# Optimization experiments

Hardware: AMD Instinct MI355X
Metric: run time of the kernel (lower is better)

Reference implementation:

```python
import jax, jax.numpy as jnp
import numpy as np

NEG = -1.0e9  # masked_fill value from the original module

def setup_inputs() -> dict:
    key = jax.random.key(0)
    kq, kk, kv, km = jax.random.split(key, 4)
    B, H, S, D = 4, 16, 2048, 64
    Q = jax.random.normal(kq, (B, H, S, D), dtype=jnp.float32)
    K = jax.random.normal(kk, (B, H, S, D), dtype=jnp.float32)
    V = jax.random.normal(kv, (B, H, S, D), dtype=jnp.float32)
    # boolean mask, True = masked out (broadcast over batch and heads)
    mask = jax.random.randint(km, (1, 1, S, S), 0, 2).astype(jnp.bool_)
    return {"Q": Q, "K": K, "V": V, "mask": mask}

def reference(Q, K, V, mask):
    d_k = K.shape[-1]
    scale = 1.0 / jnp.sqrt(jnp.asarray(d_k, dtype=Q.dtype))
    # [B,H,S,S] attention scores
    scores = jnp.einsum("bhqd,bhkd->bhqk", Q, K) * scale
    scores = jnp.where(mask, jnp.asarray(NEG, dtype=scores.dtype), scores)
    weights = jax.nn.softmax(scores, axis=-1)
    # dropout is identity in eval mode (self.training == False)
    return jnp.einsum("bhqk,bhkd->bhqd", weights, V)
```

## Files before the change

kernel.cpp:

```cpp
#include <hip/hip_runtime.h>
#include <stdint.h>

#define SQ 2048
#define DH 64

typedef __attribute__((ext_vector_type(8))) short bf16x8;
typedef __attribute__((ext_vector_type(4))) short bf16x4;
typedef __attribute__((ext_vector_type(4))) float f32x4;

static __device__ __forceinline__ unsigned short f2bf_rne(float x) {
  union { float f; uint32_t u; } v; v.f = x;
  uint32_t u = v.u;
  return (unsigned short)((u + 0x7FFFu + ((u >> 16) & 1u)) >> 16);
}

static __device__ __forceinline__ uint32_t pack_hi(float a, float b) {
  uint32_t au = __float_as_uint(a), bu = __float_as_uint(b);
#if __has_builtin(__builtin_amdgcn_perm)
  return __builtin_amdgcn_perm(bu, au, 0x07060302u);
#else
  return (bu & 0xFFFF0000u) | (au >> 16);
#endif
}

static __device__ __forceinline__ float fast_exp2(float x) {
#if __has_builtin(__builtin_amdgcn_exp2f)
  return __builtin_amdgcn_exp2f(x);
#else
  return exp2f(x);
#endif
}

#if __has_builtin(__builtin_amdgcn_mfma_f32_16x16x16_bf16)
#define MFMA_PV(a, b, c) __builtin_amdgcn_mfma_f32_16x16x16_bf16((a), (b), (c), 0, 0, 0)
#else
#define MFMA_PV(a, b, c) __builtin_amdgcn_mfma_f32_16x16x16bf16_1k((a), (b), (c), 0, 0, 0)
#endif


__global__ __launch_bounds__(256) void pack_KV(const float* __restrict__ K,
                                               const float* __restrict__ V,
                                               uint4* __restrict__ pk,
                                               uint2* __restrict__ pv) {
  __shared__ uint32_t Vw[64][33];
  const int bt = blockIdx.x;
  const int t = threadIdx.x;
  {
    const float* src = K + (size_t)bt * 64 * DH;
    uint4* dst = pk + (size_t)bt * 512;
#pragma unroll
    for (int j = 0; j < 2; ++j) {
      int i = t + j * 256;
      int kk = i >> 3, cp = i & 7;
      int c = cp ^ (kk & 7);
      const float4* s4 = (const float4*)(src + (size_t)kk * DH + c * 8);
      float4 a = s4[0], b = s4[1];
      uint4 w;
      w.x = pack_hi(a.x, a.y); w.y = pack_hi(a.z, a.w);
      w.z = pack_hi(b.x, b.y); w.w = pack_hi(b.z, b.w);
      dst[i] = w;
    }
  }
  {
    const float* src = V + (size_t)bt * 64 * DH;
#pragma unroll
    for (int half = 0; half < 2; ++half) {
      int kp = (t >> 4) + half * 16;
      int d4 = (t & 15) * 4;
      float4 a = *(const float4*)(src + (size_t)(2 * kp) * DH + d4);
      float4 b = *(const float4*)(src + (size_t)(2 * kp + 1) * DH + d4);
      Vw[d4 + 0][kp] = pack_hi(a.x, b.x);
      Vw[d4 + 1][kp] = pack_hi(a.y, b.y);
      Vw[d4 + 2][kp] = pack_hi(a.z, b.z);
      Vw[d4 + 3][kp] = pack_hi(a.w, b.w);
    }
    __syncthreads();
    uint2* dst = pv + (size_t)bt * 1024;
#pragma unroll
    for (int j = 0; j < 4; ++j) {
      int o = t + j * 256;
      int d = o >> 4, up = o & 15;
      int u = up ^ (d & 15);
      uint2 w;
      w.x = Vw[d][2 * u]; w.y = Vw[d][2 * u + 1];
      dst[o] = w;
    }
  }
}

__global__ __launch_bounds__(256) void pack_M(const int* __restrict__ mask,
                                              uint2* __restrict__ pm) {
  __shared__ uint2 Lm[16][17];
  const int qb = blockIdx.x >> 5, gb = blockIdx.x & 31;
  const int t = threadIdx.x;
  {
    int qq = t >> 4, gg = t & 15;
    int4 m = *(const int4*)(mask + (size_t)(qb * 16 + qq) * SQ + (gb * 16 + gg) * 4);
    uint2 w;
    w.x = (m.x ? 0u : 0xFFFFu) | (m.y ? 0u : 0xFFFF0000u);
    w.y = (m.z ? 0u : 0xFFFFu) | (m.w ? 0u : 0xFFFF0000u);
    Lm[gg][qq] = w;
  }
  __syncthreads();
  {
    int gg = t >> 4, qq = t & 15;
    pm[(size_t)(gb * 16 + gg) * 2048 + qb * 16 + qq] = Lm[gg][qq];
  }
}

__global__ void pack_mask_kernel(const int* __restrict__ mask,
                                 unsigned long long* __restrict__ bits) {
  const int lane = threadIdx.x & 63;
  const int gw = (blockIdx.x * blockDim.x + threadIdx.x) >> 6;
  const int nw = (gridDim.x * blockDim.x) >> 6;
  for (int w = gw; w < SQ * SQ / 64; w += nw) {
    int v = mask[(size_t)w * 64 + lane];
    unsigned long long b = __ballot(v != 0);
    if (lane == 0) bits[(size_t)(w & 31) * SQ + (w >> 5)] = b;
  }
}

__global__ __launch_bounds__(256, 4) void attn2(
    const uint4* __restrict__ pk, const uint4* __restrict__ pv,
    const uint2* __restrict__ pm, const float* __restrict__ Qg,
    float* __restrict__ Og) {
  __shared__ __align__(16) uint8_t smem[32768];

  const int id = blockIdx.x;
  const int bh = id & 63;
  const int qblk = id >> 6;
  const int t = threadIdx.x;
  const int wave = t >> 6, lane = t & 63, col = lane & 15, quad = lane >> 4;

  const float* Qb = Qg + (size_t)bh * SQ * DH;
  float* Ob = Og + (size_t)bh * SQ * DH;
  const uint4* pkb = pk + (size_t)bh * 32 * 512;
  const uint4* pvb = pv + (size_t)bh * 32 * 512;
  const int q0 = qblk * 128 + wave * 32;

  const float QSCALE = 0.18033688011112042f;
  bf16x8 qf[2][2];
#pragma unroll
  for (int s = 0; s < 2; ++s) {
    int q = q0 + s * 16 + col;
#pragma unroll
    for (int j = 0; j < 2; ++j) {
      const float4* p = (const float4*)(Qb + (size_t)q * DH + j * 32 + quad * 8);
      float4 a = p[0], b = p[1];
      bf16x8 f;
      f[0] = (short)f2bf_rne(a.x * QSCALE); f[1] = (short)f2bf_rne(a.y * QSCALE);
      f[2] = (short)f2bf_rne(a.z * QSCALE); f[3] = (short)f2bf_rne(a.w * QSCALE);
      f[4] = (short)f2bf_rne(b.x * QSCALE); f[5] = (short)f2bf_rne(b.y * QSCALE);
      f[6] = (short)f2bf_rne(b.z * QSCALE); f[7] = (short)f2bf_rne(b.w * QSCALE);
      qf[s][j] = f;
    }
  }

  const unsigned ka0 = col * 128 + ((quad ^ (col & 7)) * 16);
  const unsigned ka1 = col * 128 + (((4 + quad) ^ (col & 7)) * 16);
  unsigned va[4];
#pragma unroll
  for (int kt = 0; kt < 4; ++kt)
    va[kt] = 16384u + col * 128 + (((kt * 4 + quad) ^ col) * 8);
  const unsigned stK = t * 16;
  const unsigned stV = 16384u + t * 16;
  const size_t mqB = (size_t)(quad * 2048 + q0 + col) * 8;

  f32x4 acc[2][4];
  f32x4 accl[2];
#pragma unroll
  for (int s = 0; s < 2; ++s) {
#pragma unroll
    for (int dt = 0; dt < 4; ++dt)
#pragma unroll
      for (int r = 0; r < 4; ++r) acc[s][dt][r] = 0.0f;
#pragma unroll
    for (int r = 0; r < 4; ++r) accl[s][r] = 0.0f;
  }
  bf16x4 vones;
  vones[0] = (short)0x3F80; vones[1] = (short)0x3F80;
  vones[2] = (short)0x3F80; vones[3] = (short)0x3F80;
  const f32x4 fz = {0.0f, 0.0f, 0.0f, 0.0f};

  {
    uint4 k0 = pkb[t], k1 = pkb[t + 256];
    uint4 v0 = pvb[t], v1 = pvb[t + 256];
    *(uint4*)(smem + stK) = k0; *(uint4*)(smem + stK + 4096) = k1;
    *(uint4*)(smem + stV) = v0; *(uint4*)(smem + stV + 4096) = v1;
  }
  unsigned buf = 0;

  for (int tile = 0; tile < 32; ++tile) {
    __syncthreads();
    const int tn = (tile < 31) ? tile + 1 : 31;

    const uint4* pkt = pkb + (size_t)tn * 512;
    const uint4* pvt = pvb + (size_t)tn * 512;
    uint4 k0 = pkt[t], k1 = pkt[t + 256];
    uint4 v0 = pvt[t], v1 = pvt[t + 256];

    const char* pmt = (const char*)pm + (size_t)tile * 262144 + mqB;
    uint2 mw[2][4];
#pragma unroll
    for (int s = 0; s < 2; ++s)
#pragma unroll
      for (int kt = 0; kt < 4; ++kt)
        mw[s][kt] = *(const uint2*)(pmt + (size_t)kt * 65536 + s * 128);

    uint32_t pfw[2][4][2];
#pragma unroll
    for (int kt = 0; kt < 4; ++kt) {
      const bf16x8 kf0 = *(const bf16x8*)(smem + buf + ka0 + kt * 2048);
      const bf16x8 kf1 = *(const bf16x8*)(smem + buf + ka1 + kt * 2048);
#pragma unroll
      for (int s = 0; s < 2; ++s) {
        f32x4 st = __builtin_amdgcn_mfma_f32_16x16x32_bf16(kf0, qf[s][0], fz, 0, 0, 0);
        st = __builtin_amdgcn_mfma_f32_16x16x32_bf16(kf1, qf[s][1], st, 0, 0, 0);
        float p0 = fast_exp2(st[0]), p1 = fast_exp2(st[1]);
        float p2 = fast_exp2(st[2]), p3 = fast_exp2(st[3]);
        pfw[s][kt][0] = pack_hi(p0, p1) & mw[s][kt].x;
        pfw[s][kt][1] = pack_hi(p2, p3) & mw[s][kt].y;
      }
    }

#pragma unroll
    for (int kt = 0; kt < 4; ++kt) {
      union { uint32_t u[2]; bf16x4 v; } p0, p1;
      p0.u[0] = pfw[0][kt][0]; p0.u[1] = pfw[0][kt][1];
      p1.u[0] = pfw[1][kt][0]; p1.u[1] = pfw[1][kt][1];
      accl[0] = MFMA_PV(vones, p0.v, accl[0]);
      accl[1] = MFMA_PV(vones, p1.v, accl[1]);
#pragma unroll
      for (int dt = 0; dt < 4; ++dt) {
        union { uint2 u2; bf16x4 v; } cv;
        cv.u2 = *(const uint2*)(smem + buf + va[kt] + dt * 2048);
        acc[0][dt] = MFMA_PV(cv.v, p0.v, acc[0][dt]);
        acc[1][dt] = MFMA_PV(cv.v, p1.v, acc[1][dt]);
      }
    }

    const unsigned ob = buf ^ 8192u;
    *(uint4*)(smem + ob + stK) = k0; *(uint4*)(smem + ob + stK + 4096) = k1;
    *(uint4*)(smem + ob + stV) = v0; *(uint4*)(smem + ob + stV + 4096) = v1;
    buf = ob;
  }

#pragma unroll
  for (int s = 0; s < 2; ++s) {
    float inv = 1.0f / accl[s][0];
    int q = q0 + s * 16 + col;
    float* orow = Ob + (size_t)q * DH;
#pragma unroll
    for (int dt = 0; dt < 4; ++dt) {
      float4 o;
      o.x = acc[s][dt][0] * inv;
      o.y = acc[s][dt][1] * inv;
      o.z = acc[s][dt][2] * inv;
      o.w = acc[s][dt][3] * inv;
      *(float4*)(orow + dt * 16 + quad * 4) = o;
    }
  }
}

__global__ __launch_bounds__(512, 4) void attn_fb(
    const float* __restrict__ Qg, const float* __restrict__ Kg,
    const float* __restrict__ Vg, const unsigned long long* __restrict__ mbits,
    const int* __restrict__ mraw, float* __restrict__ Og) {
  __shared__ __align__(16) unsigned short Klds[2][64][72];
  __shared__ __align__(16) uint32_t Vtlds[2][64][36];
  const int id = blockIdx.x;
  const int bh = id & 63;
  const int qblk = id >> 6;
  const int t = threadIdx.x;
  const int wave = t >> 6, lane = t & 63, col = lane & 15, quad = lane >> 4;
  const float* Qb = Qg + (size_t)bh * SQ * DH;
  const float* Kb = Kg + (size_t)bh * SQ * DH;
  const float* Vb = Vg + (size_t)bh * SQ * DH;
  float* Ob = Og + (size_t)bh * SQ * DH;
  const int q0 = qblk * 256 + wave * 32;
  const int skk = t >> 3, sd8 = (t & 7) * 8, skp = t >> 4, sd4 = (t & 15) * 4;
  const float QSCALE = 0.18033688011112042f;
  bf16x8 qf[2][2];
#pragma unroll
  for (int s = 0; s < 2; ++s) {
    int q = q0 + s * 16 + col;
#pragma unroll
    for (int j = 0; j < 2; ++j) {
      const float4* p = (const float4*)(Qb + (size_t)q * DH + j * 32 + quad * 8);
      float4 a = p[0], b = p[1];
      bf16x8 f;
      f[0] = (short)f2bf_rne(a.x * QSCALE); f[1] = (short)f2bf_rne(a.y * QSCALE);
      f[2] = (short)f2bf_rne(a.z * QSCALE); f[3] = (short)f2bf_rne(a.w * QSCALE);
      f[4] = (short)f2bf_rne(b.x * QSCALE); f[5] = (short)f2bf_rne(b.y * QSCALE);
      f[6] = (short)f2bf_rne(b.z * QSCALE); f[7] = (short)f2bf_rne(b.w * QSCALE);
      qf[s][j] = f;
    }
  }
  f32x4 acc[2][4]; f32x4 accl[2];
#pragma unroll
  for (int s = 0; s < 2; ++s) {
#pragma unroll
    for (int dt = 0; dt < 4; ++dt)
#pragma unroll
      for (int r = 0; r < 4; ++r) acc[s][dt][r] = 0.0f;
#pragma unroll
    for (int r = 0; r < 4; ++r) accl[s][r] = 0.0f;
  }
  bf16x4 vones;
  vones[0] = (short)0x3F80; vones[1] = (short)0x3F80;
  vones[2] = (short)0x3F80; vones[3] = (short)0x3F80;
  const f32x4 fz = {0.0f, 0.0f, 0.0f, 0.0f};
  auto load_mask = [&](int ti, unsigned long long m[2]) {
    if (mbits) {
#pragma unroll
      for (int s = 0; s < 2; ++s)
        m[s] = mbits[(size_t)ti * SQ + (q0 + s * 16 + col)];
    } else {
#pragma unroll
      for (int s = 0; s < 2; ++s) {
        int q = q0 + s * 16 + col;
        unsigned long long mm = 0;
#pragma unroll
        for (int j = 0; j < 4; ++j) {
          int4 mi = *(const int4*)(mraw + (size_t)q * SQ + ti * 64 + j * 16 + quad * 4);
          unsigned long long nib = (unsigned long long)((mi.x != 0) | ((mi.y != 0) << 1) |
                                                        ((mi.z != 0) << 2) | ((mi.w != 0) << 3));
          mm |= nib << (j * 16 + quad * 4);
        }
        m[s] = mm;
      }
    }
  };
  {
    const float4* kp = (const float4*)(Kb + (size_t)skk * DH + sd8);
    float4 k0 = kp[0], k1 = kp[1];
    const float* va = Vb + (size_t)(skp * 2) * DH + sd4;
    float4 v0 = *(const float4*)va, v1 = *(const float4*)(va + DH);
    uint4 kw;
    kw.x = pack_hi(k0.x, k0.y); kw.y = pack_hi(k0.z, k0.w);
    kw.z = pack_hi(k1.x, k1.y); kw.w = pack_hi(k1.z, k1.w);
    *(uint4*)&Klds[0][skk][sd8] = kw;
    Vtlds[0][sd4 + 0][skp] = pack_hi(v0.x, v1.x);
    Vtlds[0][sd4 + 1][skp] = pack_hi(v0.y, v1.y);
    Vtlds[0][sd4 + 2][skp] = pack_hi(v0.z, v1.z);
    Vtlds[0][sd4 + 3][skp] = pack_hi(v0.w, v1.w);
  }
  unsigned long long mcur[2];
  load_mask(0, mcur);
  for (int tile = 0; tile < 32; ++tile) {
    __syncthreads();
    const int cb = tile & 1, nb = cb ^ 1;
    const int tn = (tile + 1 < 32) ? tile + 1 : tile;
    const int kkn = tn * 64;
    const float4* kp = (const float4*)(Kb + (size_t)(kkn + skk) * DH + sd8);
    float4 k0 = kp[0], k1 = kp[1];
    const float* va = Vb + (size_t)(kkn + skp * 2) * DH + sd4;
    float4 v0 = *(const float4*)va;
    float4 v1 = *(const float4*)(va + DH);
    unsigned long long mnxt[2];
    load_mask(tn, mnxt);
    uint32_t pfw[2][4][2];
#pragma unroll
    for (int kt = 0; kt < 4; ++kt) {
      const bf16x8 kf0 = *(const bf16x8*)&Klds[cb][kt * 16 + col][quad * 8];
      const bf16x8 kf1 = *(const bf16x8*)&Klds[cb][kt * 16 + col][32 + quad * 8];
#pragma unroll
      for (int s = 0; s < 2; ++s) {
        f32x4 st = __builtin_amdgcn_mfma_f32_16x16x32_bf16(kf0, qf[s][0], fz, 0, 0, 0);
        st = __builtin_amdgcn_mfma_f32_16x16x32_bf16(kf1, qf[s][1], st, 0, 0, 0);
        uint32_t nib = (uint32_t)(mcur[s] >> (kt * 16 + quad * 4)) & 0xFu;
        float p[4];
#pragma unroll
        for (int r = 0; r < 4; ++r)
          p[r] = fast_exp2(((nib >> r) & 1u) ? -1.0e9f : st[r]);
        pfw[s][kt][0] = pack_hi(p[0], p[1]);
        pfw[s][kt][1] = pack_hi(p[2], p[3]);
      }
    }
    {
      uint4 kw;
      kw.x = pack_hi(k0.x, k0.y); kw.y = pack_hi(k0.z, k0.w);
      kw.z = pack_hi(k1.x, k1.y); kw.w = pack_hi(k1.z, k1.w);
      *(uint4*)&Klds[nb][skk][sd8] = kw;
      Vtlds[nb][sd4 + 0][skp] = pack_hi(v0.x, v1.x);
      Vtlds[nb][sd4 + 1][skp] = pack_hi(v0.y, v1.y);
      Vtlds[nb][sd4 + 2][skp] = pack_hi(v0.z, v1.z);
      Vtlds[nb][sd4 + 3][skp] = pack_hi(v0.w, v1.w);
    }
    mcur[0] = mnxt[0]; mcur[1] = mnxt[1];
#pragma unroll
    for (int kt = 0; kt < 4; ++kt) {
      union { uint32_t u[2]; bf16x4 v; } p0, p1;
      p0.u[0] = pfw[0][kt][0]; p0.u[1] = pfw[0][kt][1];
      p1.u[0] = pfw[1][kt][0]; p1.u[1] = pfw[1][kt][1];
      accl[0] = MFMA_PV(vones, p0.v, accl[0]);
      accl[1] = MFMA_PV(vones, p1.v, accl[1]);
#pragma unroll
      for (int dt = 0; dt < 4; ++dt) {
        union { uint2 u2; bf16x4 v; } cv;
        cv.u2 = *(const uint2*)&Vtlds[cb][dt * 16 + col][kt * 8 + quad * 2];
        acc[0][dt] = MFMA_PV(cv.v, p0.v, acc[0][dt]);
        acc[1][dt] = MFMA_PV(cv.v, p1.v, acc[1][dt]);
      }
    }
  }
#pragma unroll
  for (int s = 0; s < 2; ++s) {
    float inv = 1.0f / accl[s][0];
    int q = q0 + s * 16 + col;
    float* orow = Ob + (size_t)q * DH;
#pragma unroll
    for (int dt = 0; dt < 4; ++dt) {
      float4 o;
      o.x = acc[s][dt][0] * inv;
      o.y = acc[s][dt][1] * inv;
      o.z = acc[s][dt][2] * inv;
      o.w = acc[s][dt][3] * inv;
      *(float4*)(orow + dt * 16 + quad * 4) = o;
    }
  }
}

extern "C" void kernel_launch(void* const* d_in, const int* in_sizes, int n_in,
                              void* d_out, int out_size, void* d_ws, size_t ws_size,
                              hipStream_t stream) {
  const float* Q = (const float*)d_in[0];
  const float* K = (const float*)d_in[1];
  const float* V = (const float*)d_in[2];
  const int* mask = (const int*)d_in[3];
  float* out = (float*)d_out;

  const size_t PK_BYTES = (size_t)64 * 32 * 8192;
  const size_t PV_BYTES = (size_t)64 * 32 * 8192;
  const size_t PM_BYTES = (size_t)512 * 2048 * 8;
  const size_t NEED = PK_BYTES + PV_BYTES + PM_BYTES;

  if (ws_size >= NEED) {
    uint4* pk = (uint4*)d_ws;
    uint2* pv = (uint2*)((char*)d_ws + PK_BYTES);
    uint2* pm = (uint2*)((char*)d_ws + PK_BYTES + PV_BYTES);
    pack_KV<<<2048, 256, 0, stream>>>(K, V, pk, (uint2*)pv);
    pack_M<<<4096, 256, 0, stream>>>(mask, pm);
    attn2<<<1024, 256, 0, stream>>>(pk, (uint4*)pv, pm, Q, out);
  } else if (ws_size >= (size_t)SQ * SQ / 8) {
    unsigned long long* bits = (unsigned long long*)d_ws;
    pack_mask_kernel<<<1024, 256, 0, stream>>>(mask, bits);
    attn_fb<<<512, 512, 0, stream>>>(Q, K, V, bits, mask, out);
  } else {
    attn_fb<<<512, 512, 0, stream>>>(Q, K, V, nullptr, mask, out);
  }
}
```

Measured before the change: 242.8 us.

## Double query rows per wave, fuse pack kernels, encode mask as perm selectors

Each wave now handles 64 query rows instead of 32, so every K/V tile loaded into shared memory is reused across twice as many rows. The grid drops to 512 blocks and launch bounds go to 2 blocks per CU to make room for the larger accumulator set. The K/V packing and mask packing kernels are merged into one launch, which removes a launch and its gap. The mask is now stored as byte-permute selectors, so a single perm instruction both packs the probabilities to bf16 and zeroes masked entries, replacing a pack followed by an AND. The risks are higher register pressure and lower occupancy, and a 512-block grid may not fill every CU evenly.

```diff
diff --git a/kernel.cpp b/kernel.cpp
--- a/kernel.cpp
+++ b/kernel.cpp
@@ -23,6 +23,21 @@
 #endif
 }
 
+static __device__ __forceinline__ uint32_t pack_sel(float a, float b, uint32_t sel) {
+#if __has_builtin(__builtin_amdgcn_perm)
+  return __builtin_amdgcn_perm(__float_as_uint(b), __float_as_uint(a), sel);
+#else
+  uint32_t r = 0;
+  uint64_t src = ((uint64_t)__float_as_uint(b) << 32) | __float_as_uint(a);
+  for (int i = 0; i < 4; ++i) {
+    uint32_t sb = (sel >> (8 * i)) & 0xFF;
+    uint32_t byte = (sb < 8) ? (uint32_t)((src >> (8 * sb)) & 0xFF) : 0u;
+    r |= byte << (8 * i);
+  }
+  return r;
+#endif
+}
+
 static __device__ __forceinline__ float fast_exp2(float x) {
 #if __has_builtin(__builtin_amdgcn_exp2f)
   return __builtin_amdgcn_exp2f(x);
@@ -37,74 +52,74 @@
 #define MFMA_PV(a, b, c) __builtin_amdgcn_mfma_f32_16x16x16bf16_1k((a), (b), (c), 0, 0, 0)
 #endif
 
-
-__global__ __launch_bounds__(256) void pack_KV(const float* __restrict__ K,
-                                               const float* __restrict__ V,
-                                               uint4* __restrict__ pk,
-                                               uint2* __restrict__ pv) {
-  __shared__ uint32_t Vw[64][33];
-  const int bt = blockIdx.x;
+__global__ __launch_bounds__(256) void pack_all(const float* __restrict__ K,
+                                                const float* __restrict__ V,
+                                                const int* __restrict__ mask,
+                                                uint4* __restrict__ pk,
+                                                uint2* __restrict__ pv,
+                                                uint2* __restrict__ pm) {
   const int t = threadIdx.x;
-  {
-    const float* src = K + (size_t)bt * 64 * DH;
-    uint4* dst = pk + (size_t)bt * 512;
-#pragma unroll
-    for (int j = 0; j < 2; ++j) {
-      int i = t + j * 256;
-      int kk = i >> 3, cp = i & 7;
-      int c = cp ^ (kk & 7);
-      const float4* s4 = (const float4*)(src + (size_t)kk * DH + c * 8);
-      float4 a = s4[0], b = s4[1];
-      uint4 w;
-      w.x = pack_hi(a.x, a.y); w.y = pack_hi(a.z, a.w);
-      w.z = pack_hi(b.x, b.y); w.w = pack_hi(b.z, b.w);
-      dst[i] = w;
-    }
-  }
-  {
-    const float* src = V + (size_t)bt * 64 * DH;
-#pragma unroll
-    for (int half = 0; half < 2; ++half) {
-      int kp = (t >> 4) + half * 16;
-      int d4 = (t & 15) * 4;
-      float4 a = *(const float4*)(src + (size_t)(2 * kp) * DH + d4);
-      float4 b = *(const float4*)(src + (size_t)(2 * kp + 1) * DH + d4);
-      Vw[d4 + 0][kp] = pack_hi(a.x, b.x);
-      Vw[d4 + 1][kp] = pack_hi(a.y, b.y);
-      Vw[d4 + 2][kp] = pack_hi(a.z, b.z);
-      Vw[d4 + 3][kp] = pack_hi(a.w, b.w);
+  if (blockIdx.x < 2048) {
+    __shared__ uint32_t Vw[64][33];
+    const int bt = blockIdx.x;
+    {
+      const float* src = K + (size_t)bt * 64 * DH;
+      uint4* dst = pk + (size_t)bt * 512;
+#pragma unroll
+      for (int j = 0; j < 2; ++j) {
+        int i = t + j * 256;
+        int kk = i >> 3, cp = i & 7;
+        int c = cp ^ (kk & 7);
+        const float4* s4 = (const float4*)(src + (size_t)kk * DH + c * 8);
+        float4 a = s4[0], b = s4[1];
+        uint4 w;
+        w.x = pack_hi(a.x, a.y); w.y = pack_hi(a.z, a.w);
+        w.z = pack_hi(b.x, b.y); w.w = pack_hi(b.z, b.w);
+        dst[i] = w;
+      }
+    }
+    {
+      const float* src = V + (size_t)bt * 64 * DH;
+#pragma unroll
+      for (int half = 0; half < 2; ++half) {
+        int kp = (t >> 4) + half * 16;
+        int d4 = (t & 15) * 4;
+        float4 a = *(const float4*)(src + (size_t)(2 * kp) * DH + d4);
+        float4 b = *(const float4*)(src + (size_t)(2 * kp + 1) * DH + d4);
+        Vw[d4 + 0][kp] = pack_hi(a.x, b.x);
+        Vw[d4 + 1][kp] = pack_hi(a.y, b.y);
+        Vw[d4 + 2][kp] = pack_hi(a.z, b.z);
+        Vw[d4 + 3][kp] = pack_hi(a.w, b.w);
+      }
+      __syncthreads();
+      uint2* dst = pv + (size_t)bt * 1024;
+#pragma unroll
+      for (int j = 0; j < 4; ++j) {
+        int o = t + j * 256;
+        int d = o >> 4, up = o & 15;
+        int u = up ^ (d & 15);
+        uint2 w;
+        w.x = Vw[d][2 * u]; w.y = Vw[d][2 * u + 1];
+        dst[o] = w;
+      }
+    }
+  } else {
+    __shared__ uint2 Lm[16][17];
+    const int bid = blockIdx.x - 2048;
+    const int qb = bid >> 5, gb = bid & 31;
+    {
+      int qq = t >> 4, gg = t & 15;
+      int4 m = *(const int4*)(mask + (size_t)(qb * 16 + qq) * SQ + (gb * 64 + gg * 4));
+      uint2 w;
+      w.x = (m.x ? 0x00000C0Cu : 0x00000302u) | (m.y ? 0x0C0C0000u : 0x07060000u);
+      w.y = (m.z ? 0x00000C0Cu : 0x00000302u) | (m.w ? 0x0C0C0000u : 0x07060000u);
+      Lm[gg][qq] = w;
     }
     __syncthreads();
-    uint2* dst = pv + (size_t)bt * 1024;
-#pragma unroll
-    for (int j = 0; j < 4; ++j) {
-      int o = t + j * 256;
-      int d = o >> 4, up = o & 15;
-      int u = up ^ (d & 15);
-      uint2 w;
-      w.x = Vw[d][2 * u]; w.y = Vw[d][2 * u + 1];
-      dst[o] = w;
-    }
-  }
-}
-
-__global__ __launch_bounds__(256) void pack_M(const int* __restrict__ mask,
-                                              uint2* __restrict__ pm) {
-  __shared__ uint2 Lm[16][17];
-  const int qb = blockIdx.x >> 5, gb = blockIdx.x & 31;
-  const int t = threadIdx.x;
-  {
-    int qq = t >> 4, gg = t & 15;
-    int4 m = *(const int4*)(mask + (size_t)(qb * 16 + qq) * SQ + (gb * 16 + gg) * 4);
-    uint2 w;
-    w.x = (m.x ? 0u : 0xFFFFu) | (m.y ? 0u : 0xFFFF0000u);
-    w.y = (m.z ? 0u : 0xFFFFu) | (m.w ? 0u : 0xFFFF0000u);
-    Lm[gg][qq] = w;
-  }
-  __syncthreads();
-  {
-    int gg = t >> 4, qq = t & 15;
-    pm[(size_t)(gb * 16 + gg) * 2048 + qb * 16 + qq] = Lm[gg][qq];
+    {
+      int gg = t >> 4, qq = t & 15;
+      pm[(size_t)(gb * 16 + gg) * 2048 + qb * 16 + qq] = Lm[gg][qq];
+    }
   }
 }
 
@@ -120,7 +135,7 @@
   }
 }
 
-__global__ __launch_bounds__(256, 4) void attn2(
+__global__ __launch_bounds__(256, 2) void attn3(
     const uint4* __restrict__ pk, const uint4* __restrict__ pv,
     const uint2* __restrict__ pm, const float* __restrict__ Qg,
     float* __restrict__ Og) {
@@ -136,12 +151,12 @@
   float* Ob = Og + (size_t)bh * SQ * DH;
   const uint4* pkb = pk + (size_t)bh * 32 * 512;
   const uint4* pvb = pv + (size_t)bh * 32 * 512;
-  const int q0 = qblk * 128 + wave * 32;
+  const int q0 = qblk * 256 + wave * 64;
 
   const float QSCALE = 0.18033688011112042f;
-  bf16x8 qf[2][2];
-#pragma unroll
-  for (int s = 0; s < 2; ++s) {
+  bf16x8 qf[4][2];
+#pragma unroll
+  for (int s = 0; s < 4; ++s) {
     int q = q0 + s * 16 + col;
 #pragma unroll
     for (int j = 0; j < 2; ++j) {
@@ -164,12 +179,12 @@
     va[kt] = 16384u + col * 128 + (((kt * 4 + quad) ^ col) * 8);
   const unsigned stK = t * 16;
   const unsigned stV = 16384u + t * 16;
-  const size_t mqB = (size_t)(quad * 2048 + q0 + col) * 8;
-
-  f32x4 acc[2][4];
-  f32x4 accl[2];
-#pragma unroll
-  for (int s = 0; s < 2; ++s) {
+  const char* pmt = (const char*)pm + (size_t)(quad * 2048 + q0 + col) * 8;
+
+  f32x4 acc[4][4];
+  f32x4 accl[4];
+#pragma unroll
+  for (int s = 0; s < 4; ++s) {
 #pragma unroll
     for (int dt = 0; dt < 4; ++dt)
 #pragma unroll
@@ -199,43 +214,38 @@
     uint4 k0 = pkt[t], k1 = pkt[t + 256];
     uint4 v0 = pvt[t], v1 = pvt[t + 256];
 
-    const char* pmt = (const char*)pm + (size_t)tile * 262144 + mqB;
-    uint2 mw[2][4];
-#pragma unroll
-    for (int s = 0; s < 2; ++s)
-#pragma unroll
-      for (int kt = 0; kt < 4; ++kt)
-        mw[s][kt] = *(const uint2*)(pmt + (size_t)kt * 65536 + s * 128);
-
-    uint32_t pfw[2][4][2];
 #pragma unroll
     for (int kt = 0; kt < 4; ++kt) {
-      const bf16x8 kf0 = *(const bf16x8*)(smem + buf + ka0 + kt * 2048);
-      const bf16x8 kf1 = *(const bf16x8*)(smem + buf + ka1 + kt * 2048);
-#pragma unroll
-      for (int s = 0; s < 2; ++s) {
+      const bf16x8 kf0 = *(const bf16x8*)(smem + buf + kt * 2048 + ka0);
+      const bf16x8 kf1 = *(const bf16x8*)(smem + buf + kt * 2048 + ka1);
+      uint2 mw[4];
+#pragma unroll
+      for (int s = 0; s < 4; ++s)
+        mw[s] = *(const uint2*)(pmt + (size_t)kt * 65536 + s * 128);
+
+      uint32_t pf[4][2];
+#pragma unroll
+      for (int s = 0; s < 4; ++s) {
         f32x4 st = __builtin_amdgcn_mfma_f32_16x16x32_bf16(kf0, qf[s][0], fz, 0, 0, 0);
         st = __builtin_amdgcn_mfma_f32_16x16x32_bf16(kf1, qf[s][1], st, 0, 0, 0);
         float p0 = fast_exp2(st[0]), p1 = fast_exp2(st[1]);
         float p2 = fast_exp2(st[2]), p3 = fast_exp2(st[3]);
-        pfw[s][kt][0] = pack_hi(p0, p1) & mw[s][kt].x;
-        pfw[s][kt][1] = pack_hi(p2, p3) & mw[s][kt].y;
-      }
-    }
-
-#pragma unroll
-    for (int kt = 0; kt < 4; ++kt) {
-      union { uint32_t u[2]; bf16x4 v; } p0, p1;
-      p0.u[0] = pfw[0][kt][0]; p0.u[1] = pfw[0][kt][1];
-      p1.u[0] = pfw[1][kt][0]; p1.u[1] = pfw[1][kt][1];
-      accl[0] = MFMA_PV(vones, p0.v, accl[0]);
-      accl[1] = MFMA_PV(vones, p1.v, accl[1]);
-#pragma unroll
-      for (int dt = 0; dt < 4; ++dt) {
-        union { uint2 u2; bf16x4 v; } cv;
-        cv.u2 = *(const uint2*)(smem + buf + va[kt] + dt * 2048);
-        acc[0][dt] = MFMA_PV(cv.v, p0.v, acc[0][dt]);
-        acc[1][dt] = MFMA_PV(cv.v, p1.v, acc[1][dt]);
+        pf[s][0] = pack_sel(p0, p1, mw[s].x);
+        pf[s][1] = pack_sel(p2, p3, mw[s].y);
+      }
+
+      union { uint2 u2; bf16x4 v; } vf[4];
+#pragma unroll
+      for (int dt = 0; dt < 4; ++dt)
+        vf[dt].u2 = *(const uint2*)(smem + buf + va[kt] + dt * 2048);
+#pragma unroll
+      for (int s = 0; s < 4; ++s) {
+        union { uint32_t u[2]; bf16x4 v; } pw;
+        pw.u[0] = pf[s][0]; pw.u[1] = pf[s][1];
+        accl[s] = MFMA_PV(vones, pw.v, accl[s]);
+#pragma unroll
+        for (int dt = 0; dt < 4; ++dt)
+          acc[s][dt] = MFMA_PV(vf[dt].v, pw.v, acc[s][dt]);
       }
     }
 
@@ -243,10 +253,11 @@
     *(uint4*)(smem + ob + stK) = k0; *(uint4*)(smem + ob + stK + 4096) = k1;
     *(uint4*)(smem + ob + stV) = v0; *(uint4*)(smem + ob + stV + 4096) = v1;
     buf = ob;
-  }
-
-#pragma unroll
-  for (int s = 0; s < 2; ++s) {
+    pmt += 262144;
+  }
+
+#pragma unroll
+  for (int s = 0; s < 4; ++s) {
     float inv = 1.0f / accl[s][0];
     int q = q0 + s * 16 + col;
     float* orow = Ob + (size_t)q * DH;
@@ -439,9 +450,8 @@
     uint4* pk = (uint4*)d_ws;
     uint2* pv = (uint2*)((char*)d_ws + PK_BYTES);
     uint2* pm = (uint2*)((char*)d_ws + PK_BYTES + PV_BYTES);
-    pack_KV<<<2048, 256, 0, stream>>>(K, V, pk, (uint2*)pv);
-    pack_M<<<4096, 256, 0, stream>>>(mask, pm);
-    attn2<<<1024, 256, 0, stream>>>(pk, (uint4*)pv, pm, Q, out);
+    pack_all<<<6144, 256, 0, stream>>>(K, V, mask, pk, pv, pm);
+    attn3<<<512, 256, 0, stream>>>(pk, (uint4*)pv, pm, Q, out);
   } else if (ws_size >= (size_t)SQ * SQ / 8) {
     unsigned long long* bits = (unsigned long long*)d_ws;
     pack_mask_kernel<<<1024, 256, 0, stream>>>(mask, bits);
```

Result: no change. 242.7 us (-0.0%).
